# Kernel optimization log

Measured on AMD Instinct MI355X. Metric: run time of the kernel, lower is better.

Reference implementation:

```python
import jax, jax.numpy as jnp
import numpy as np

DE = 4   # encoder depth (de); ne+1 == de so all cells are used
DD = 4   # decoder depth (dd)
BS = 64
SL = 256
FL = 256
SI = 512
SH = 512  # must equal SI (original module requires it)


def setup_inputs() -> dict:
    key = jax.random.key(0)
    ks = jax.random.split(key, 8)
    s = 0.05  # init scale to keep gates out of saturation
    z4 = (DE, BS, SH)
    inp = {
        "x": jax.random.normal(ks[0], (BS, SL, SI), jnp.float32),
        "fl": FL,
        # gate order along last dim: [f, i, g, o], each of width SH
        "enc_W": jax.random.normal(ks[1], (DE, DE, SH, 4 * SH), jnp.float32) * s,
        "enc_V": jax.random.normal(ks[2], (DE, DE, SH, 4 * SH), jnp.float32) * s,
        "enc_b": jnp.zeros((DE, DE, 4 * SH), jnp.float32),
        "enc_h0": jnp.zeros(z4, jnp.float32),
        "enc_c0": jnp.zeros(z4, jnp.float32),
        "dec_W": jax.random.normal(ks[3], (DD, DD, SH, 4 * SH), jnp.float32) * s,
        "dec_V": jax.random.normal(ks[4], (DD, DD, SH, 4 * SH), jnp.float32) * s,
        "dec_b": jnp.zeros((DD, DD, 4 * SH), jnp.float32),
        "dec_h0": jnp.zeros((DD, BS, SH), jnp.float32),
        "dec_c0": jnp.zeros((DD, BS, SH), jnp.float32),
        "fin_W": jax.random.normal(ks[5], (SH, SI), jnp.float32) * s,
        "fin_b": jnp.zeros((SI,), jnp.float32),
    }
    return inp


def _lstm_cell(W, V, b, x, h, c):
    # fused gate GEMM: z = x@U + h@Vh + b, gates [f,i,g,o]
    z = x @ W + h @ V + b                      # (bs, 4*sh)
    f, i, g, o = jnp.split(z, 4, axis=-1)
    f = jax.nn.sigmoid(f)
    i = jax.nn.sigmoid(i)
    g = jnp.tanh(g)
    o = jax.nn.sigmoid(o)
    C = f * c + i * g
    H = o * jnp.tanh(C)
    return H, C


def _forward(x, fl, enc_W, enc_V, enc_b, enc_h0, enc_c0,
             dec_W, dec_V, dec_b, dec_h0, dec_c0, fin_W, fin_b):
    de = enc_W.shape[0]
    dd = dec_W.shape[0]

    def enc_step(carry, x_t):
        h, c = carry                            # (de, bs, sh) each
        for L in range(de):                     # over the de ModuleLists
            for e in range(de):                 # cells 0..de-1 within a list
                inp = x_t if e == 0 else h[e - 1]
                H, C = _lstm_cell(enc_W[L, e], enc_V[L, e], enc_b[L, e], inp, h[e], c[e])
                h = h.at[e].set(H)
                c = c.at[e].set(C)
        return (h, c), None

    (h_enc, _), _ = jax.lax.scan(enc_step, (enc_h0, enc_c0), jnp.swapaxes(x, 0, 1))
    state0 = h_enc[de - 1]                      # last updated encoder hidden

    def dec_step(carry, _):
        h, c, state = carry
        outs = []
        for L in range(dd):
            for e in range(dd):
                inp = state if e == 0 else h[e - 1]
                H, C = _lstm_cell(dec_W[L, e], dec_V[L, e], dec_b[L, e], inp, h[e], c[e])
                h = h.at[e].set(H)
                c = c.at[e].set(C)
            state = h[dd - 1]
            outs.append(state)                  # output appended per list, per step
        return (h, c, state), jnp.stack(outs)   # (dd, bs, sh)

    _, ys = jax.lax.scan(dec_step, (dec_h0, dec_c0, state0), None, length=fl)
    # ys: (fl, dd, bs, sh) -> (fl*dd, bs, sh) -> (bs, fl*dd, sh)
    out = ys.reshape(fl * dd, ys.shape[2], ys.shape[3]).transpose(1, 0, 2)
    return jax.nn.sigmoid(out @ fin_W + fin_b)  # (bs, fl*dd, si)


def reference(x, fl, enc_W, enc_V, enc_b, enc_h0, enc_c0,
              dec_W, dec_V, dec_b, dec_h0, dec_c0, fin_W, fin_b):
    return _forward(x, fl, enc_W, enc_V, enc_b, enc_h0, enc_c0,
                    dec_W, dec_V, dec_b, dec_h0, dec_c0, fin_W, fin_b)
```

## Files before the change

kernel.cpp:

```cpp
#include <hip/hip_runtime.h>

typedef _Float16 f16;
typedef _Float16 f16x8 __attribute__((ext_vector_type(8)));
typedef float f32x4 __attribute__((ext_vector_type(4)));

#define BS 64
#define SL 256
#define FL 256
#define SI 512
#define SH 512
#define NBLK 256
#define TFULL 1028

__device__ __forceinline__ float sigmoidf_(float x) { return 1.f / (1.f + __expf(-x)); }
__device__ __forceinline__ float tanhf_(float x) { float e = __expf(2.f * x); return 1.f - 2.f / (e + 1.f); }

__device__ __forceinline__ f16x8 ldg_cohere(const f16* p) {
  f16x8 r;
  asm volatile("global_load_dwordx4 %0, %1, off sc0 sc1"
               : "=v"(r) : "v"(p) : "memory");
  return r;
}

__global__ void conv_w(const float* __restrict__ W, const float* __restrict__ V,
                       f16* __restrict__ out) {
  long idx = (long)blockIdx.x * blockDim.x + threadIdx.x;
  int j    = (int)(idx & 7);
  int lane = (int)((idx >> 3) & 63);
  int kk   = (int)((idx >> 9) & 15);
  int kh   = (int)((idx >> 13) & 1);
  int g    = (int)((idx >> 14) & 3);
  int nt   = (int)((idx >> 16) & 31);
  long cell = idx >> 21;
  int n = g * 512 + nt * 16 + (lane & 15);
  int k = kh * 512 + kk * 32 + (lane >> 4) * 8 + j;
  float v = (k < 512) ? W[(cell * 512 + k) * 2048 + n]
                      : V[(cell * 512 + (k - 512)) * 2048 + n];
  out[idx] = (f16)v;
}

__global__ void conv_x(const float* __restrict__ x, f16* __restrict__ xt) {
  long idx = (long)blockIdx.x * blockDim.x + threadIdx.x;
  int i = (int)(idx & 511);
  int b = (int)((idx >> 9) & 63);
  int t = (int)(idx >> 15);
  xt[idx] = (f16)x[((long)b * SL + t) * SI + i];
}

__global__ void conv_fin(const float* __restrict__ finW, f16* __restrict__ fint) {
  long idx = (long)blockIdx.x * blockDim.x + threadIdx.x;
  int k = (int)(idx & 511);
  int n = (int)(idx >> 9);
  fint[idx] = (f16)finW[(long)k * SI + n];
}

__global__ void init_state(const float* __restrict__ h0e, const float* __restrict__ h0d,
                           f16* __restrict__ h_enc, f16* __restrict__ h_dec) {
  long idx = (long)blockIdx.x * blockDim.x + threadIdx.x;
  f16 he = (f16)h0e[idx];
  h_enc[idx] = he;
  h_enc[idx + 131072] = he;
  h_dec[idx + 131072] = (f16)h0d[idx];
}

__device__ __forceinline__ void store_h_agent(f16* p, float v) {
  f16 h = (f16)v;
  __hip_atomic_store((unsigned short*)p, __builtin_bit_cast(unsigned short, h),
                     __ATOMIC_RELAXED, __HIP_MEMORY_SCOPE_AGENT);
}

#define SWZ(ROW, BOFF) (((ROW) << 10) + ((BOFF) ^ ((((ROW) & 7)) << 4)))

#define VMCNT0() do {                                                             \
    asm volatile("s_waitcnt vmcnt(0)" ::: "memory");                              \
    __builtin_amdgcn_sched_barrier(0);                                            \
  } while (0)

#define RAWBAR() do {                                                             \
    asm volatile("s_waitcnt lgkmcnt(0)" ::: "memory");                            \
    __builtin_amdgcn_sched_barrier(0);                                            \
    __builtin_amdgcn_s_barrier();                                                 \
    __builtin_amdgcn_sched_barrier(0);                                            \
  } while (0)

#define WAVE_ORDER() do {                                                          \
    asm volatile("s_waitcnt vmcnt(16)" ::: "memory");                              \
    __builtin_amdgcn_sched_barrier(0);                                             \
  } while (0)

#define END_STEP_ENC(TARGET) do {                                                  \
    __builtin_amdgcn_s_barrier();                                                  \
    asm volatile("" ::: "memory");                                                 \
    if (tid == 0)                                                                  \
      __hip_atomic_store(&bar[bflag], (TARGET), __ATOMIC_RELAXED,                  \
                         __HIP_MEMORY_SCOPE_AGENT);                                \
    if (wid == 0) {                                                                \
      for (;;) {                                                                   \
        int a0 = __hip_atomic_load(&bar[pe0], __ATOMIC_RELAXED,                    \
                                   __HIP_MEMORY_SCOPE_AGENT);                      \
        int a1 = __hip_atomic_load(&bar[pe1], __ATOMIC_RELAXED,                    \
                                   __HIP_MEMORY_SCOPE_AGENT);                      \
        if (a0 >= (TARGET) && a1 >= (TARGET)) break;                               \
        __builtin_amdgcn_s_sleep(1);                                               \
      }                                                                            \
    }                                                                              \
    __builtin_amdgcn_s_barrier();                                                  \
    asm volatile("" ::: "memory");                                                 \
    __builtin_amdgcn_sched_barrier(0);                                             \
  } while (0)

#define END_STEP_DEC(TARGET) do {                                                  \
    __builtin_amdgcn_s_barrier();                                                  \
    asm volatile("" ::: "memory");                                                 \
    if (tid == 0)                                                                  \
      __hip_atomic_store(&bar[bflag], (TARGET), __ATOMIC_RELAXED,                  \
                         __HIP_MEMORY_SCOPE_AGENT);                                \
    if (wid == 0) {                                                                \
      while (__hip_atomic_load(&bar[pd], __ATOMIC_RELAXED,                         \
                               __HIP_MEMORY_SCOPE_AGENT) < (TARGET))               \
        __builtin_amdgcn_s_sleep(1);                                               \
    }                                                                              \
    __builtin_amdgcn_s_barrier();                                                  \
    asm volatile("" ::: "memory");                                                 \
    __builtin_amdgcn_sched_barrier(0);                                             \
  } while (0)

#define END_STEP_FULL(TARGET) do {                                                 \
    __builtin_amdgcn_s_barrier();                                                  \
    asm volatile("" ::: "memory");                                                 \
    if (tid == 0)                                                                  \
      __hip_atomic_store(&bar[bflag], (TARGET), __ATOMIC_RELAXED,                  \
                         __HIP_MEMORY_SCOPE_AGENT);                                \
    if (wid == 0) {                                                                \
      for (;;) {                                                                   \
        int a0 = __hip_atomic_load(&bar[pf0], __ATOMIC_RELAXED,                    \
                                   __HIP_MEMORY_SCOPE_AGENT);                      \
        int a1 = __hip_atomic_load(&bar[pf1], __ATOMIC_RELAXED,                    \
                                   __HIP_MEMORY_SCOPE_AGENT);                      \
        int a2 = __hip_atomic_load(&bar[pf2], __ATOMIC_RELAXED,                    \
                                   __HIP_MEMORY_SCOPE_AGENT);                      \
        int a3 = __hip_atomic_load(&bar[pf3], __ATOMIC_RELAXED,                    \
                                   __HIP_MEMORY_SCOPE_AGENT);                      \
        if (a0 >= (TARGET) && a1 >= (TARGET) && a2 >= (TARGET) && a3 >= (TARGET))  \
          break;                                                                   \
        __builtin_amdgcn_s_sleep(2);                                               \
      }                                                                            \
    }                                                                              \
    __builtin_amdgcn_s_barrier();                                                  \
    asm volatile("" ::: "memory");                                                 \
    __builtin_amdgcn_sched_barrier(0);                                             \
  } while (0)

#define ENC_BODY(DD, P, TARGET) do {                                               \
    const int v = (DD) - eslot;                                                    \
    if (v >= 0 && v < 1024) {                                                      \
      const int L = v & 3, t = v >> 2;                                             \
      const f16* inp = (eslot == 0) ? (xt + (long)t * HSz)                         \
                                    : (h_enc + ((P)*4 + (eslot - 1)) * HSz);       \
      const f16* hin = h_enc + ((P)*4 + eslot) * HSz;                              \
      f16* hout = h_enc + ((1 - (P))*4 + eslot) * HSz;                             \
      {        \
        const f16* c0p = inp + emt * 16384;                                        \
        const f16* c1p = hin + emt * 16384;                                        \
        f16x8 tr[8];                                                               \
        _Pragma("unroll")                                                          \
        for (int k2 = 0; k2 < 4; ++k2) {                                           \
          const int s = tid + k2 * 512, row = s >> 6, c16 = s & 63;                \
          tr[k2]     = ldg_cohere(c0p + row * 512 + c16 * 8);                      \
          tr[k2 + 4] = ldg_cohere(c1p + row * 512 + c16 * 8);                      \
        }                                                                          \
        VMCNT0();                                                                  \
        _Pragma("unroll")                                                          \
        for (int k2 = 0; k2 < 4; ++k2) {                                           \
          const int s = tid + k2 * 512, row = s >> 6, c16 = s & 63;                \
          *(f16x8*)(AsBuf + SWZ(row, c16 * 16)) = tr[k2];                          \
          *(f16x8*)(AsBuf + 32768 + SWZ(row, c16 * 16)) = tr[k2 + 4];              \
        }                                                                          \
      }                                                                            \
      RAWBAR();                                                                    \
      f32x4 acc0 = 0.f, acc1 = 0.f;                                                \
      _Pragma("unroll")                                                            \
      for (int kk = 0; kk < 16; ++kk) {                                            \
        f16x8 a0 = *(const f16x8*)(AsBuf + kh * 32768 +                            \
                                   SWZ(col, kk * 64 + kg * 16));                   \
        f16x8 a1 = *(const f16x8*)(AsBuf + kh * 32768 +                            \
                                   SWZ(col + 16, kk * 64 + kg * 16));              \
        acc0 = __builtin_amdgcn_mfma_f32_16x16x32_f16(a0, B[kk], acc0, 0,0,0);     \
        acc1 = __builtin_amdgcn_mfma_f32_16x16x32_f16(a1, B[kk], acc1, 0,0,0);     \
      }                                                                            \
      _Pragma("unroll")                                                            \
      for (int r = 0; r < 4; ++r) {                                                \
        zred[wid][kg*4 + r][col] = acc0[r];                                        \
        zred[wid][16 + kg*4 + r][col] = acc1[r];                                   \
      }                                                                            \
      RAWBAR();                                                                    \
      {                                                                            \
        const int row = tid >> 4, ci = tid & 15, n = n0 + ci;                      \
        const float* bl = bias_enc_lds + L * 64 + ci;                              \
        float zf = bl[0]  + zred[0][row][ci] + zred[4][row][ci];                   \
        float zi = bl[16] + zred[1][row][ci] + zred[5][row][ci];                   \
        float zg = bl[32] + zred[2][row][ci] + zred[6][row][ci];                   \
        float zo = bl[48] + zred[3][row][ci] + zred[7][row][ci];                   \
        float f_ = sigmoidf_(zf), i_ = sigmoidf_(zi);                              \
        float g_ = tanhf_(zg),   o_ = sigmoidf_(zo);                               \
        const int grow = emt * 32 + row;                                           \
        float cin = (v == 0) ? enc_c0[(long)eslot * HSz + grow * SH + n] : ce;     \
        float cc = f_ * cin + i_ * g_;                                             \
        ce = cc;                                                                   \
        store_h_agent(hout + grow * SH + n, o_ * tanhf_(cc));                      \
      }                                                                            \
      const f16* wn = (v + 1 < 1024)                                               \
          ? wt_enc + ((long)(((v + 1) & 3) * 4 + eslot) << 21) + wslice            \
          : wt_dec + wslice;                                                       \
      asm volatile("" ::: "memory");                                               \
      _Pragma("unroll")                                                            \
      for (int kk = 0; kk < 16; ++kk) B[kk] = *(const f16x8*)(wn + kk * 512);      \
      WAVE_ORDER();                                                                \
    }                                                                              \
    END_STEP_ENC(TARGET);                                                          \
  } while (0)

#define DEC_BODY(E, CD, TARGET) do {                                               \
    const f16* inp;                                                                \
    if ((E) == 0)                                                                  \
      inp = (vv == 0) ? state0 : h_dec + ((par ^ 1) * 4 + 3) * HSz;                \
    else                                                                           \
      inp = h_dec + (par * 4 + (E) - 1) * HSz;                                     \
    const f16* hin = h_dec + ((par ^ 1) * 4 + (E)) * HSz;                          \
    f16* hout = h_dec + (par * 4 + (E)) * HSz;                                     \
    {                                                                              \
      const int drow = tid >> 6, dc16 = tid & 63;                                  \
      f16x8 t0 = ldg_cohere(inp + dmt * 4096 + drow * 512 + dc16 * 8);             \
      f16x8 t1 = ldg_cohere(hin + dmt * 4096 + drow * 512 + dc16 * 8);             \
      VMCNT0();                                                                    \
      *(f16x8*)(AsBuf + SWZ(drow, dc16 * 16)) = t0;                                \
      *(f16x8*)(AsBuf + 8192 + SWZ(drow, dc16 * 16)) = t1;                         \
    }                                                                              \
    RAWBAR();                                                                      \
    f32x4 acc = 0.f;                                                               \
    _Pragma("unroll")                                                              \
    for (int kk = 0; kk < 16; ++kk) {                                              \
      f16x8 a = *(const f16x8*)(AsBuf + kh * 8192 +                                \
                                SWZ(col & 7, kk * 64 + kg * 16));                  \
      acc = __builtin_amdgcn_mfma_f32_16x16x32_f16(a, B[kk], acc, 0,0,0);          \
    }                                                                              \
    if (kg < 2) {                                                                  \
      _Pragma("unroll")                                                            \
      for (int r = 0; r < 4; ++r) zred[wid][kg*4 + r][col] = acc[r];               \
    }                                                                              \
    RAWBAR();                                                                      \
    if (tid < 128) {                                                               \
      const int row = tid >> 4, ci = tid & 15, n = n0 + ci;                        \
      const float* bl = bias_dec_lds + (L * 4 + (E)) * 64 + ci;                    \
      float zf = bl[0]  + zred[0][row][ci] + zred[4][row][ci];                     \
      float zi = bl[16] + zred[1][row][ci] + zred[5][row][ci];                     \
      float zg = bl[32] + zred[2][row][ci] + zred[6][row][ci];                     \
      float zo = bl[48] + zred[3][row][ci] + zred[7][row][ci];                     \
      float f_ = sigmoidf_(zf), i_ = sigmoidf_(zi);                                \
      float g_ = tanhf_(zg),   o_ = sigmoidf_(zo);                                 \
      const int grow = dmt * 8 + row;                                              \
      float cin = (vv == 0) ? dec_c0[(long)(E) * HSz + grow * SH + n] : CD;        \
      float cc = f_ * cin + i_ * g_;                                               \
      CD = cc;                                                                     \
      float hv = o_ * tanhf_(cc);                                                  \
      store_h_agent(hout + grow * SH + n, hv);                                     \
      if ((E) == 3) ys[((long)grow * 1024 + vv) * SH + n] = (f16)hv;               \
    }                                                                              \
    {                                                                              \
      const int Lp = ((E) < 3) ? L : ((vv + 1) & 3);                               \
      const int Ep = ((E) + 1) & 3;                                                \
      const f16* wn = wt_dec + ((long)(Lp * 4 + Ep) << 21) + wslice;               \
      asm volatile("" ::: "memory");                                               \
      _Pragma("unroll")                                                            \
      for (int kk = 0; kk < 16; ++kk) B[kk] = *(const f16x8*)(wn + kk * 512);      \
      WAVE_ORDER();                                                                \
    }                                                                              \
    END_STEP_DEC(TARGET);                                                          \
  } while (0)

__global__ __launch_bounds__(512, 2) void lstm_persist(
    const f16* __restrict__ xt,
    const f16* __restrict__ wt_enc, const f16* __restrict__ wt_dec,
    const float* __restrict__ enc_b, const float* __restrict__ dec_b,
    const float* __restrict__ enc_c0, const float* __restrict__ dec_c0,
    f16* __restrict__ h_enc, f16* __restrict__ h_dec,
    f16* __restrict__ ys, int* __restrict__ bar) {
  const int tid = threadIdx.x;
  const int lane = tid & 63;
  const int wid = tid >> 6;
  const int g = wid & 3;
  const int kh = wid >> 2;
  const int col = lane & 15;
  const int kg = lane >> 4;
  const int idx = blockIdx.x;
  const int nt = idx & 31;
  const int n0 = nt << 4;
  const int eslot = idx >> 6;
  const int emt = (idx >> 5) & 1;
  const int dmt = idx >> 5;

  const int bflag = idx * 32;
  const int pe0 = ((((lane) >> 5) << 6) | (emt << 5) | (lane & 31)) * 32;
  const int pe1 = (((((lane + 64)) >> 5) << 6) | (emt << 5) | ((lane + 64) & 31)) * 32;
  const int pd = (dmt * 32 + (lane & 31)) * 32;
  const int pf0 = (lane * 4 + 0) * 32;
  const int pf1 = (lane * 4 + 1) * 32;
  const int pf2 = (lane * 4 + 2) * 32;
  const int pf3 = (lane * 4 + 3) * 32;

  __shared__ __align__(16) char AsBuf[65536];
  __shared__ float zred[8][32][17];
  __shared__ float bias_enc_lds[4 * 4 * 16];
  __shared__ float bias_dec_lds[16 * 4 * 16];

  const long wslice = ((long)(nt * 4 + g) * 2 + kh) * 8192 + lane * 8;
  const int HSz = BS * SH;
  const f16* const state0 = h_enc + (1 * 4 + 3) * HSz;

  for (int i = tid; i < 256; i += 512) {
    int L = i >> 6, gg = (i >> 4) & 3, ci = i & 15;
    bias_enc_lds[i] = enc_b[(L * 4 + eslot) * 2048 + gg * 512 + n0 + ci];
  }
  for (int i = tid; i < 1024; i += 512) {
    int cell = i >> 6, gg = (i >> 4) & 3, ci = i & 15;
    bias_dec_lds[i] = dec_b[cell * 2048 + gg * 512 + n0 + ci];
  }

  f16x8 B[16];
  {
    const f16* w = wt_enc + ((long)eslot << 21) + wslice;
#pragma unroll
    for (int kk = 0; kk < 16; ++kk) B[kk] = *(const f16x8*)(w + kk * 512);
  }
  __syncthreads();

  float ce = 0.f;
  float cd0 = 0.f, cd1 = 0.f, cd2 = 0.f, cd3 = 0.f;

  for (int d = 0;; d += 2) {
    ENC_BODY(d, 0, d + 1);
    if (d == 1026) break;
    ENC_BODY(d + 1, 1, d + 2);
  }

  END_STEP_FULL(TFULL);

  for (int vv = 0; vv < 1024; ++vv) {
    const int L = vv & 3, par = vv & 1;
    DEC_BODY(0, cd0, TFULL + vv * 4 + 1);
    DEC_BODY(1, cd1, TFULL + vv * 4 + 2);
    DEC_BODY(2, cd2, TFULL + vv * 4 + 3);
    DEC_BODY(3, cd3, TFULL + vv * 4 + 4);
  }
}

__global__ __launch_bounds__(256) void final_gemm(const f16* __restrict__ ys,
                                                  const f16* __restrict__ fint,
                                                  const float* __restrict__ finb,
                                                  float* __restrict__ out) {
  const int lane = threadIdx.x & 63;
  const int w = threadIdx.x >> 6;
  const int col = lane & 15;
  const int kg = lane >> 4;
  const long m0 = (long)blockIdx.y * 64;
  const int n0 = (blockIdx.x * 4 + w) * 16;

  f32x4 acc[4];
#pragma unroll
  for (int mi = 0; mi < 4; ++mi) acc[mi] = 0.f;

#pragma unroll 2
  for (int kk = 0; kk < 16; ++kk) {
    f16x8 b = *(const f16x8*)(fint + (long)(n0 + col) * 512 + kk * 32 + kg * 8);
#pragma unroll
    for (int mi = 0; mi < 4; ++mi) {
      f16x8 a = *(const f16x8*)(ys + (m0 + mi * 16 + col) * 512 + kk * 32 + kg * 8);
      acc[mi] = __builtin_amdgcn_mfma_f32_16x16x32_f16(a, b, acc[mi], 0, 0, 0);
    }
  }
  const int n = n0 + col;
  const float bn = finb[n];
#pragma unroll
  for (int mi = 0; mi < 4; ++mi)
#pragma unroll
    for (int r = 0; r < 4; ++r)
      out[(m0 + mi * 16 + kg * 4 + r) * 512 + n] = sigmoidf_(acc[mi][r] + bn);
}

extern "C" void kernel_launch(void* const* d_in, const int* in_sizes, int n_in,
                              void* d_out, int out_size, void* d_ws, size_t ws_size,
                              hipStream_t stream) {
  const float* x      = (const float*)d_in[0];
  const float* enc_W  = (const float*)d_in[2];
  const float* enc_V  = (const float*)d_in[3];
  const float* enc_b  = (const float*)d_in[4];
  const float* enc_h0 = (const float*)d_in[5];
  const float* enc_c0 = (const float*)d_in[6];
  const float* dec_W  = (const float*)d_in[7];
  const float* dec_V  = (const float*)d_in[8];
  const float* dec_b  = (const float*)d_in[9];
  const float* dec_h0 = (const float*)d_in[10];
  const float* dec_c0 = (const float*)d_in[11];
  const float* fin_W  = (const float*)d_in[12];
  const float* fin_b  = (const float*)d_in[13];
  float* out = (float*)d_out;

  f16* wt_enc = (f16*)d_ws;
  f16* wt_dec = wt_enc + (long)16 * 2048 * 1024;
  f16* xt     = wt_dec + (long)16 * 2048 * 1024;
  f16* fint   = xt + (long)SL * BS * SI;
  f16* ys     = fint + (long)SH * SI;
  f16* h_enc  = ys + (long)BS * (FL * 4) * SH;
  f16* h_dec  = h_enc + (long)2 * 4 * BS * SH;
  float* c_unused = (float*)(h_dec + (long)2 * 4 * BS * SH);
  int* bar = (int*)(c_unused + (long)8 * BS * SH);

  hipMemsetAsync(bar, 0, 65536, stream);

  conv_w<<<131072, 256, 0, stream>>>(enc_W, enc_V, wt_enc);
  conv_w<<<131072, 256, 0, stream>>>(dec_W, dec_V, wt_dec);
  conv_x<<<32768, 256, 0, stream>>>(x, xt);
  conv_fin<<<1024, 256, 0, stream>>>(fin_W, fint);
  init_state<<<512, 256, 0, stream>>>(enc_h0, dec_h0, h_enc, h_dec);

  lstm_persist<<<NBLK, 512, 0, stream>>>(xt, wt_enc, wt_dec, enc_b, dec_b,
                                         enc_c0, dec_c0, h_enc, h_dec, ys, bar);

  dim3 fg(8, 1024);
  final_gemm<<<fg, 256, 0, stream>>>(ys, fint, fin_b, out);
}
```

Measured before the change: 20.50 ms.

## Replace decoder flag barriers with tagged hidden-state packets and split-K per wave

The decoder phase stops using per-step global flag barriers. Each block now publishes its hidden-state slice as 16-byte packets that carry a step tag in the last word, and consumers spin on those packets directly until the tags match. This merges data transfer and synchronisation into one load and removes the separate flag round trip. The decoder GEMM is also rearranged so each wave covers a K-slice for all four gates, with an 8-way LDS reduction. The cost is 25% padding overhead in the packed format, extra pack and unpack work, and spin-polling traffic on the data itself.

Result: slower. 24.77 ms, median of 3 (+20.8%).

```diff
diff --git a/kernel.cpp b/kernel.cpp
--- a/kernel.cpp
+++ b/kernel.cpp
@@ -3,6 +3,9 @@
 typedef _Float16 f16;
 typedef _Float16 f16x8 __attribute__((ext_vector_type(8)));
 typedef float f32x4 __attribute__((ext_vector_type(4)));
+typedef unsigned int u32;
+typedef u32 u32x4 __attribute__((ext_vector_type(4)));
+typedef u32 u32x2 __attribute__((ext_vector_type(2)));
 
 #define BS 64
 #define SL 256
@@ -10,16 +13,23 @@
 #define SI 512
 #define SH 512
 #define NBLK 256
-#define TFULL 1028
+#define SLAB 6144
 
 __device__ __forceinline__ float sigmoidf_(float x) { return 1.f / (1.f + __expf(-x)); }
 __device__ __forceinline__ float tanhf_(float x) { float e = __expf(2.f * x); return 1.f - 2.f / (e + 1.f); }
 
 __device__ __forceinline__ f16x8 ldg_cohere(const f16* p) {
   f16x8 r;
-  asm volatile("global_load_dwordx4 %0, %1, off sc0 sc1"
-               : "=v"(r) : "v"(p) : "memory");
+  asm volatile("global_load_dwordx4 %0, %1, off sc0 sc1" : "=v"(r) : "v"(p) : "memory");
   return r;
+}
+__device__ __forceinline__ u32x4 ldg_tag(const u32x4* p) {
+  u32x4 r;
+  asm volatile("global_load_dwordx4 %0, %1, off sc0 sc1" : "=v"(r) : "v"(p) : "memory");
+  return r;
+}
+__device__ __forceinline__ void stg_tag(u32x4* p, u32x4 v) {
+  asm volatile("global_store_dwordx4 %0, %1, off sc0 sc1" :: "v"(p), "v"(v) : "memory");
 }
 
 __global__ void conv_w(const float* __restrict__ W, const float* __restrict__ V,
@@ -54,13 +64,32 @@
   fint[idx] = (f16)finW[(long)k * SI + n];
 }
 
-__global__ void init_state(const float* __restrict__ h0e, const float* __restrict__ h0d,
-                           f16* __restrict__ h_enc, f16* __restrict__ h_dec) {
+__global__ void init_state(const float* __restrict__ h0e, f16* __restrict__ h_enc) {
   long idx = (long)blockIdx.x * blockDim.x + threadIdx.x;
   f16 he = (f16)h0e[idx];
   h_enc[idx] = he;
   h_enc[idx + 131072] = he;
-  h_dec[idx + 131072] = (f16)h0d[idx];
+}
+
+__global__ void init_dec_tags(const float* __restrict__ h0d, u32x4* __restrict__ hdt) {
+  int i = blockIdx.x * blockDim.x + threadIdx.x;
+  int E = i / 6144;
+  int r = i - E * 6144;
+  int row = r / 96;
+  int rem = r - row * 96;
+  int unt = rem / 3;
+  int u = rem - unt * 3;
+  int c0 = unt * 16 + u * 6;
+  const float* src = h0d + (long)E * 32768 + row * 512 + c0;
+  u32 d[3] = {0, 0, 0};
+  int count = (u == 2) ? 4 : 6;
+  for (int k = 0; k < count; k += 2) {
+    f16 a = (f16)src[k], b = (f16)src[k + 1];
+    d[k >> 1] = (u32)__builtin_bit_cast(unsigned short, a) |
+                ((u32)__builtin_bit_cast(unsigned short, b) << 16);
+  }
+  u32x4 val = {d[0], d[1], d[2], (u32)(4 + E)};
+  hdt[(4 + E) * SLAB + r] = val;
 }
 
 __device__ __forceinline__ void store_h_agent(f16* p, float v) {
@@ -109,48 +138,6 @@
     __builtin_amdgcn_sched_barrier(0);                                             \
   } while (0)
 
-#define END_STEP_DEC(TARGET) do {                                                  \
-    __builtin_amdgcn_s_barrier();                                                  \
-    asm volatile("" ::: "memory");                                                 \
-    if (tid == 0)                                                                  \
-      __hip_atomic_store(&bar[bflag], (TARGET), __ATOMIC_RELAXED,                  \
-                         __HIP_MEMORY_SCOPE_AGENT);                                \
-    if (wid == 0) {                                                                \
-      while (__hip_atomic_load(&bar[pd], __ATOMIC_RELAXED,                         \
-                               __HIP_MEMORY_SCOPE_AGENT) < (TARGET))               \
-        __builtin_amdgcn_s_sleep(1);                                               \
-    }                                                                              \
-    __builtin_amdgcn_s_barrier();                                                  \
-    asm volatile("" ::: "memory");                                                 \
-    __builtin_amdgcn_sched_barrier(0);                                             \
-  } while (0)
-
-#define END_STEP_FULL(TARGET) do {                                                 \
-    __builtin_amdgcn_s_barrier();                                                  \
-    asm volatile("" ::: "memory");                                                 \
-    if (tid == 0)                                                                  \
-      __hip_atomic_store(&bar[bflag], (TARGET), __ATOMIC_RELAXED,                  \
-                         __HIP_MEMORY_SCOPE_AGENT);                                \
-    if (wid == 0) {                                                                \
-      for (;;) {                                                                   \
-        int a0 = __hip_atomic_load(&bar[pf0], __ATOMIC_RELAXED,                    \
-                                   __HIP_MEMORY_SCOPE_AGENT);                      \
-        int a1 = __hip_atomic_load(&bar[pf1], __ATOMIC_RELAXED,                    \
-                                   __HIP_MEMORY_SCOPE_AGENT);                      \
-        int a2 = __hip_atomic_load(&bar[pf2], __ATOMIC_RELAXED,                    \
-                                   __HIP_MEMORY_SCOPE_AGENT);                      \
-        int a3 = __hip_atomic_load(&bar[pf3], __ATOMIC_RELAXED,                    \
-                                   __HIP_MEMORY_SCOPE_AGENT);                      \
-        if (a0 >= (TARGET) && a1 >= (TARGET) && a2 >= (TARGET) && a3 >= (TARGET))  \
-          break;                                                                   \
-        __builtin_amdgcn_s_sleep(2);                                               \
-      }                                                                            \
-    }                                                                              \
-    __builtin_amdgcn_s_barrier();                                                  \
-    asm volatile("" ::: "memory");                                                 \
-    __builtin_amdgcn_sched_barrier(0);                                             \
-  } while (0)
-
 #define ENC_BODY(DD, P, TARGET) do {                                               \
     const int v = (DD) - eslot;                                                    \
     if (v >= 0 && v < 1024) {                                                      \
@@ -159,20 +146,20 @@
                                     : (h_enc + ((P)*4 + (eslot - 1)) * HSz);       \
       const f16* hin = h_enc + ((P)*4 + eslot) * HSz;                              \
       f16* hout = h_enc + ((1 - (P))*4 + eslot) * HSz;                             \
-      {        \
+      {                                                                            \
         const f16* c0p = inp + emt * 16384;                                        \
         const f16* c1p = hin + emt * 16384;                                        \
         f16x8 tr[8];                                                               \
         _Pragma("unroll")                                                          \
         for (int k2 = 0; k2 < 4; ++k2) {                                           \
-          const int s = tid + k2 * 512, row = s >> 6, c16 = s & 63;                \
+          const int s2 = tid + k2 * 512, row = s2 >> 6, c16 = s2 & 63;             \
           tr[k2]     = ldg_cohere(c0p + row * 512 + c16 * 8);                      \
           tr[k2 + 4] = ldg_cohere(c1p + row * 512 + c16 * 8);                      \
         }                                                                          \
         VMCNT0();                                                                  \
         _Pragma("unroll")                                                          \
         for (int k2 = 0; k2 < 4; ++k2) {                                           \
-          const int s = tid + k2 * 512, row = s >> 6, c16 = s & 63;                \
+          const int s2 = tid + k2 * 512, row = s2 >> 6, c16 = s2 & 63;             \
           *(f16x8*)(AsBuf + SWZ(row, c16 * 16)) = tr[k2];                          \
           *(f16x8*)(AsBuf + 32768 + SWZ(row, c16 * 16)) = tr[k2 + 4];              \
         }                                                                          \
@@ -190,28 +177,48 @@
       }                                                                            \
       _Pragma("unroll")                                                            \
       for (int r = 0; r < 4; ++r) {                                                \
-        zred[wid][kg*4 + r][col] = acc0[r];                                        \
-        zred[wid][16 + kg*4 + r][col] = acc1[r];                                   \
+        zredE[wid][kg*4 + r][col] = acc0[r];                                       \
+        zredE[wid][16 + kg*4 + r][col] = acc1[r];                                  \
       }                                                                            \
       RAWBAR();                                                                    \
+      const bool s0f = (v == 1023) && (eslot == 3);                                \
       {                                                                            \
         const int row = tid >> 4, ci = tid & 15, n = n0 + ci;                      \
         const float* bl = bias_enc_lds + L * 64 + ci;                              \
-        float zf = bl[0]  + zred[0][row][ci] + zred[4][row][ci];                   \
-        float zi = bl[16] + zred[1][row][ci] + zred[5][row][ci];                   \
-        float zg = bl[32] + zred[2][row][ci] + zred[6][row][ci];                   \
-        float zo = bl[48] + zred[3][row][ci] + zred[7][row][ci];                   \
+        float zf = bl[0]  + zredE[0][row][ci] + zredE[4][row][ci];                 \
+        float zi = bl[16] + zredE[1][row][ci] + zredE[5][row][ci];                 \
+        float zg = bl[32] + zredE[2][row][ci] + zredE[6][row][ci];                 \
+        float zo = bl[48] + zredE[3][row][ci] + zredE[7][row][ci];                 \
         float f_ = sigmoidf_(zf), i_ = sigmoidf_(zi);                              \
         float g_ = tanhf_(zg),   o_ = sigmoidf_(zo);                               \
         const int grow = emt * 32 + row;                                           \
         float cin = (v == 0) ? enc_c0[(long)eslot * HSz + grow * SH + n] : ce;     \
         float cc = f_ * cin + i_ * g_;                                             \
         ce = cc;                                                                   \
-        store_h_agent(hout + grow * SH + n, o_ * tanhf_(cc));                      \
+        float hv = o_ * tanhf_(cc);                                                \
+        store_h_agent(hout + grow * SH + n, hv);                                   \
+        if (s0f) pb16[row * 16 + ci] = (f16)hv;                                    \
+      }                                                                            \
+      if (s0f) {                                                                   \
+        RAWBAR();                                                                  \
+        if (tid < 96) {                                                            \
+          int u = tid % 3, rowp = tid / 3;                                         \
+          const char* pbc = (const char*)pb16 + rowp * 32;                         \
+          u32 d0, d1, d2;                                                          \
+          if (u == 0) { u32x2 t2 = *(const u32x2*)(pbc);                           \
+                        d0 = t2.x; d1 = t2.y; d2 = *(const u32*)(pbc + 8); }       \
+          else if (u == 1) { d0 = *(const u32*)(pbc + 12);                         \
+                             u32x2 t2 = *(const u32x2*)(pbc + 16);                 \
+                             d1 = t2.x; d2 = t2.y; }                               \
+          else { u32x2 t2 = *(const u32x2*)(pbc + 24);                             \
+                 d0 = t2.x; d1 = t2.y; d2 = 0; }                                   \
+          u32x4 val = {d0, d1, d2, 7u};                                            \
+          stg_tag(s0t + (emt * 32 + rowp) * 96 + nt * 3 + u, val);                 \
+        }                                                                          \
       }                                                                            \
       const f16* wn = (v + 1 < 1024)                                               \
           ? wt_enc + ((long)(((v + 1) & 3) * 4 + eslot) << 21) + wslice            \
-          : wt_dec + wslice;                                                       \
+          : wt_enc + wslice;                                                       \
       asm volatile("" ::: "memory");                                               \
       _Pragma("unroll")                                                            \
       for (int kk = 0; kk < 16; ++kk) B[kk] = *(const f16x8*)(wn + kk * 512);      \
@@ -220,70 +227,12 @@
     END_STEP_ENC(TARGET);                                                          \
   } while (0)
 
-#define DEC_BODY(E, CD, TARGET) do {                                               \
-    const f16* inp;                                                                \
-    if ((E) == 0)                                                                  \
-      inp = (vv == 0) ? state0 : h_dec + ((par ^ 1) * 4 + 3) * HSz;                \
-    else                                                                           \
-      inp = h_dec + (par * 4 + (E) - 1) * HSz;                                     \
-    const f16* hin = h_dec + ((par ^ 1) * 4 + (E)) * HSz;                          \
-    f16* hout = h_dec + (par * 4 + (E)) * HSz;                                     \
-    {                                                                              \
-      const int drow = tid >> 6, dc16 = tid & 63;                                  \
-      f16x8 t0 = ldg_cohere(inp + dmt * 4096 + drow * 512 + dc16 * 8);             \
-      f16x8 t1 = ldg_cohere(hin + dmt * 4096 + drow * 512 + dc16 * 8);             \
-      VMCNT0();                                                                    \
-      *(f16x8*)(AsBuf + SWZ(drow, dc16 * 16)) = t0;                                \
-      *(f16x8*)(AsBuf + 8192 + SWZ(drow, dc16 * 16)) = t1;                         \
-    }                                                                              \
-    RAWBAR();                                                                      \
-    f32x4 acc = 0.f;                                                               \
-    _Pragma("unroll")                                                              \
-    for (int kk = 0; kk < 16; ++kk) {                                              \
-      f16x8 a = *(const f16x8*)(AsBuf + kh * 8192 +                                \
-                                SWZ(col & 7, kk * 64 + kg * 16));                  \
-      acc = __builtin_amdgcn_mfma_f32_16x16x32_f16(a, B[kk], acc, 0,0,0);          \
-    }                                                                              \
-    if (kg < 2) {                                                                  \
-      _Pragma("unroll")                                                            \
-      for (int r = 0; r < 4; ++r) zred[wid][kg*4 + r][col] = acc[r];               \
-    }                                                                              \
-    RAWBAR();                                                                      \
-    if (tid < 128) {                                                               \
-      const int row = tid >> 4, ci = tid & 15, n = n0 + ci;                        \
-      const float* bl = bias_dec_lds + (L * 4 + (E)) * 64 + ci;                    \
-      float zf = bl[0]  + zred[0][row][ci] + zred[4][row][ci];                     \
-      float zi = bl[16] + zred[1][row][ci] + zred[5][row][ci];                     \
-      float zg = bl[32] + zred[2][row][ci] + zred[6][row][ci];                     \
-      float zo = bl[48] + zred[3][row][ci] + zred[7][row][ci];                     \
-      float f_ = sigmoidf_(zf), i_ = sigmoidf_(zi);                                \
-      float g_ = tanhf_(zg),   o_ = sigmoidf_(zo);                                 \
-      const int grow = dmt * 8 + row;                                              \
-      float cin = (vv == 0) ? dec_c0[(long)(E) * HSz + grow * SH + n] : CD;        \
-      float cc = f_ * cin + i_ * g_;                                               \
-      CD = cc;                                                                     \
-      float hv = o_ * tanhf_(cc);                                                  \
-      store_h_agent(hout + grow * SH + n, hv);                                     \
-      if ((E) == 3) ys[((long)grow * 1024 + vv) * SH + n] = (f16)hv;               \
-    }                                                                              \
-    {                                                                              \
-      const int Lp = ((E) < 3) ? L : ((vv + 1) & 3);                               \
-      const int Ep = ((E) + 1) & 3;                                                \
-      const f16* wn = wt_dec + ((long)(Lp * 4 + Ep) << 21) + wslice;               \
-      asm volatile("" ::: "memory");                                               \
-      _Pragma("unroll")                                                            \
-      for (int kk = 0; kk < 16; ++kk) B[kk] = *(const f16x8*)(wn + kk * 512);      \
-      WAVE_ORDER();                                                                \
-    }                                                                              \
-    END_STEP_DEC(TARGET);                                                          \
-  } while (0)
-
 __global__ __launch_bounds__(512, 2) void lstm_persist(
     const f16* __restrict__ xt,
     const f16* __restrict__ wt_enc, const f16* __restrict__ wt_dec,
     const float* __restrict__ enc_b, const float* __restrict__ dec_b,
     const float* __restrict__ enc_c0, const float* __restrict__ dec_c0,
-    f16* __restrict__ h_enc, f16* __restrict__ h_dec,
+    f16* __restrict__ h_enc, u32x4* __restrict__ hdt, u32x4* __restrict__ s0t,
     f16* __restrict__ ys, int* __restrict__ bar) {
   const int tid = threadIdx.x;
   const int lane = tid & 63;
@@ -302,20 +251,16 @@
   const int bflag = idx * 32;
   const int pe0 = ((((lane) >> 5) << 6) | (emt << 5) | (lane & 31)) * 32;
   const int pe1 = (((((lane + 64)) >> 5) << 6) | (emt << 5) | ((lane + 64) & 31)) * 32;
-  const int pd = (dmt * 32 + (lane & 31)) * 32;
-  const int pf0 = (lane * 4 + 0) * 32;
-  const int pf1 = (lane * 4 + 1) * 32;
-  const int pf2 = (lane * 4 + 2) * 32;
-  const int pf3 = (lane * 4 + 3) * 32;
 
   __shared__ __align__(16) char AsBuf[65536];
-  __shared__ float zred[8][32][17];
-  __shared__ float bias_enc_lds[4 * 4 * 16];
-  __shared__ float bias_dec_lds[16 * 4 * 16];
+  __shared__ float zredE[8][32][17];
+  __shared__ float zredD[8][4][8][17];
+  __shared__ float bias_enc_lds[256];
+  __shared__ float bias_dec_lds[1024];
+  __shared__ __align__(16) f16 pb16[512];
 
   const long wslice = ((long)(nt * 4 + g) * 2 + kh) * 8192 + lane * 8;
   const int HSz = BS * SH;
-  const f16* const state0 = h_enc + (1 * 4 + 3) * HSz;
 
   for (int i = tid; i < 256; i += 512) {
     int L = i >> 6, gg = (i >> 4) & 3, ci = i & 15;
@@ -343,14 +288,131 @@
     ENC_BODY(d + 1, 1, d + 2);
   }
 
-  END_STEP_FULL(TFULL);
-
-  for (int vv = 0; vv < 1024; ++vv) {
-    const int L = vv & 3, par = vv & 1;
-    DEC_BODY(0, cd0, TFULL + vv * 4 + 1);
-    DEC_BODY(1, cd1, TFULL + vv * 4 + 2);
-    DEC_BODY(2, cd2, TFULL + vv * 4 + 3);
-    DEC_BODY(3, cd3, TFULL + vv * 4 + 4);
+#pragma unroll
+  for (int g2 = 0; g2 < 4; ++g2)
+#pragma unroll
+    for (int kkl = 0; kkl < 4; ++kkl)
+      B[g2 * 4 + kkl] = *(const f16x8*)(wt_dec +
+          ((long)(nt * 4 + g2) * 2 + kh) * 8192 + (g * 4 + kkl) * 512 + lane * 8);
+
+  for (int s = 0; s < 4096; ++s) {
+    const int vv = s >> 2, E = s & 3, par = vv & 1, L = vv & 3;
+    const u32 T = 8u + (u32)s;
+    const u32x4* inpT;
+    if (E > 0) inpT = hdt + (par * 4 + E - 1) * SLAB;
+    else if (vv > 0) inpT = hdt + ((par ^ 1) * 4 + 3) * SLAB;
+    else inpT = s0t;
+    const u32x4* hinT = hdt + ((par ^ 1) * 4 + E) * SLAB;
+
+    {
+      const int q1 = tid + 512;
+      const int c1 = (q1 >= 768);
+      const int l0 = tid, l1 = q1 - (c1 ? 768 : 0), l2 = tid + 256;
+      const u32x4* a0 = inpT + dmt * 768 + l0;
+      const u32x4* a1 = (c1 ? hinT : inpT) + dmt * 768 + l1;
+      const u32x4* a2 = hinT + dmt * 768 + l2;
+      const u32 e0 = T - 1, e1 = c1 ? T - 4 : T - 1, e2 = T - 4;
+      u32x4 r0, r1, r2;
+      for (;;) {
+        r0 = ldg_tag(a0); r1 = ldg_tag(a1); r2 = ldg_tag(a2);
+        VMCNT0();
+        if (r0.w == e0 && r1.w == e1 && r2.w == e2) break;
+        __builtin_amdgcn_s_sleep(2);
+      }
+      const u32x4 rr[3] = {r0, r1, r2};
+      const int ll[3] = {l0, l1, l2};
+      const int cc3[3] = {0, c1, 1};
+#pragma unroll
+      for (int j = 0; j < 3; ++j) {
+        int row = ll[j] / 96;
+        int rem = ll[j] - row * 96;
+        int unt = rem / 3;
+        int u = rem - unt * 3;
+        char* A = AsBuf + cc3[j] * 8192 + SWZ(row, unt * 32);
+        char* B2 = AsBuf + cc3[j] * 8192 + SWZ(row, unt * 32 + 16);
+        u32x4 r = rr[j];
+        if (u == 0) { u32x2 t2 = {r.x, r.y}; *(u32x2*)A = t2; *(u32*)(A + 8) = r.z; }
+        else if (u == 1) { *(u32*)(A + 12) = r.x; u32x2 t2 = {r.y, r.z}; *(u32x2*)B2 = t2; }
+        else { u32x2 t2 = {r.x, r.y}; *(u32x2*)(B2 + 8) = t2; }
+      }
+    }
+    RAWBAR();
+
+    f16x8 a_[4];
+#pragma unroll
+    for (int kkl = 0; kkl < 4; ++kkl)
+      a_[kkl] = *(const f16x8*)(AsBuf + kh * 8192 +
+                                SWZ(col & 7, g * 256 + kkl * 64 + kg * 16));
+    f32x4 accg0 = 0.f, accg1 = 0.f, accg2 = 0.f, accg3 = 0.f;
+#pragma unroll
+    for (int kkl = 0; kkl < 4; ++kkl) {
+      accg0 = __builtin_amdgcn_mfma_f32_16x16x32_f16(a_[kkl], B[0 * 4 + kkl], accg0, 0,0,0);
+      accg1 = __builtin_amdgcn_mfma_f32_16x16x32_f16(a_[kkl], B[1 * 4 + kkl], accg1, 0,0,0);
+      accg2 = __builtin_amdgcn_mfma_f32_16x16x32_f16(a_[kkl], B[2 * 4 + kkl], accg2, 0,0,0);
+      accg3 = __builtin_amdgcn_mfma_f32_16x16x32_f16(a_[kkl], B[3 * 4 + kkl], accg3, 0,0,0);
+    }
+    if (kg < 2) {
+#pragma unroll
+      for (int r = 0; r < 4; ++r) {
+        zredD[wid][0][kg * 4 + r][col] = accg0[r];
+        zredD[wid][1][kg * 4 + r][col] = accg1[r];
+        zredD[wid][2][kg * 4 + r][col] = accg2[r];
+        zredD[wid][3][kg * 4 + r][col] = accg3[r];
+      }
+    }
+    if (s + 1 < 4096) {
+      const int s2 = s + 1;
+      const long cell2 = (long)((((s2 >> 2) & 3) * 4) + (s2 & 3));
+      const f16* wb = wt_dec + (cell2 << 21);
+      asm volatile("" ::: "memory");
+#pragma unroll
+      for (int g2 = 0; g2 < 4; ++g2)
+#pragma unroll
+        for (int kkl = 0; kkl < 4; ++kkl)
+          B[g2 * 4 + kkl] = *(const f16x8*)(wb +
+              ((long)(nt * 4 + g2) * 2 + kh) * 8192 + (g * 4 + kkl) * 512 + lane * 8);
+    }
+    RAWBAR();
+
+    if (tid < 128) {
+      const int row = tid >> 4, ci = tid & 15, n = n0 + ci;
+      const float* bl = bias_dec_lds + (L * 4 + E) * 64 + ci;
+      float zf = bl[0], zi = bl[16], zg = bl[32], zo = bl[48];
+#pragma unroll
+      for (int w = 0; w < 8; ++w) {
+        zf += zredD[w][0][row][ci];
+        zi += zredD[w][1][row][ci];
+        zg += zredD[w][2][row][ci];
+        zo += zredD[w][3][row][ci];
+      }
+      float f_ = sigmoidf_(zf), i_ = sigmoidf_(zi);
+      float g_ = tanhf_(zg),   o_ = sigmoidf_(zo);
+      float cin;
+      if (vv == 0) cin = dec_c0[(long)E * HSz + (dmt * 8 + row) * SH + n];
+      else cin = (E == 0) ? cd0 : (E == 1) ? cd1 : (E == 2) ? cd2 : cd3;
+      float cc = f_ * cin + i_ * g_;
+      if (E == 0) cd0 = cc; else if (E == 1) cd1 = cc;
+      else if (E == 2) cd2 = cc; else cd3 = cc;
+      float hv = o_ * tanhf_(cc);
+      pb16[row * 16 + ci] = (f16)hv;
+      if (E == 3) ys[((long)(dmt * 8 + row) * 1024 + vv) * SH + n] = (f16)hv;
+    }
+    RAWBAR();
+
+    if (tid < 24) {
+      const int u = tid % 3, rowp = tid / 3;
+      const char* pbc = (const char*)pb16 + rowp * 32;
+      u32 d0, d1, d2;
+      if (u == 0) { u32x2 t2 = *(const u32x2*)(pbc);
+                    d0 = t2.x; d1 = t2.y; d2 = *(const u32*)(pbc + 8); }
+      else if (u == 1) { d0 = *(const u32*)(pbc + 12);
+                         u32x2 t2 = *(const u32x2*)(pbc + 16);
+                         d1 = t2.x; d2 = t2.y; }
+      else { u32x2 t2 = *(const u32x2*)(pbc + 24);
+             d0 = t2.x; d1 = t2.y; d2 = 0; }
+      u32x4 val = {d0, d1, d2, T};
+      stg_tag(hdt + (par * 4 + E) * SLAB + (dmt * 8 + rowp) * 96 + nt * 3 + u, val);
+    }
   }
 }
 
@@ -411,20 +473,24 @@
   f16* fint   = xt + (long)SL * BS * SI;
   f16* ys     = fint + (long)SH * SI;
   f16* h_enc  = ys + (long)BS * (FL * 4) * SH;
-  f16* h_dec  = h_enc + (long)2 * 4 * BS * SH;
-  float* c_unused = (float*)(h_dec + (long)2 * 4 * BS * SH);
+  f16* h_unused = h_enc + (long)2 * 4 * BS * SH;
+  float* c_unused = (float*)(h_unused + (long)2 * 4 * BS * SH);
   int* bar = (int*)(c_unused + (long)8 * BS * SH);
+  u32x4* hdt = (u32x4*)((char*)bar + 65536);
+  u32x4* s0t = hdt + 8 * SLAB;
 
   hipMemsetAsync(bar, 0, 65536, stream);
+  hipMemsetAsync(hdt, 0, (size_t)(8 * SLAB + SLAB) * 16, stream);
 
   conv_w<<<131072, 256, 0, stream>>>(enc_W, enc_V, wt_enc);
   conv_w<<<131072, 256, 0, stream>>>(dec_W, dec_V, wt_dec);
   conv_x<<<32768, 256, 0, stream>>>(x, xt);
   conv_fin<<<1024, 256, 0, stream>>>(fin_W, fint);
-  init_state<<<512, 256, 0, stream>>>(enc_h0, dec_h0, h_enc, h_dec);
+  init_state<<<512, 256, 0, stream>>>(enc_h0, h_enc);
+  init_dec_tags<<<96, 256, 0, stream>>>(dec_h0, hdt);
 
   lstm_persist<<<NBLK, 512, 0, stream>>>(xt, wt_enc, wt_dec, enc_b, dec_b,
-                                         enc_c0, dec_c0, h_enc, h_dec, ys, bar);
+                                         enc_c0, dec_c0, h_enc, hdt, s0t, ys, bar);
 
   dim3 fg(8, 1024);
   final_gemm<<<fg, 256, 0, stream>>>(ys, fint, fin_b, out);
```
